# Kernel tuning notes

Measured on AMD Instinct MI355X. Metric: run time of the kernel, lower is better.

## Reference

```python
import jax, jax.numpy as jnp
import numpy as np

TIME_NUM, WEEK_NUM = 288, 7
HID = 32          # hid_dim
T_OUT, IN_DIM = 12, 3
RF_DIM = 64       # random_feature_dim
TAU = 1.0
EPS_RF = 1e-6
EPS_LN = 1e-5


def _make_proj(m, d, seed=0):
    """Performer random matrix: stacked rows of QR-orthogonalized dxd blocks,
    scaled by chi-distributed row norms (create_random_matrix, scaling=0)."""
    rng = np.random.RandomState(seed)
    blocks = []
    for _ in range(m // d):
        q, _ = np.linalg.qr(rng.randn(d, d))
        blocks.append(q.T)
    rem = m - (m // d) * d
    if rem > 0:
        q, _ = np.linalg.qr(rng.randn(d, d))
        blocks.append(q.T[:rem])
    mat = np.vstack(blocks)
    mult = np.linalg.norm(rng.randn(m, d), axis=1)
    return jnp.asarray((mult[:, None] * mat).astype(np.float32))


def setup_inputs() -> dict:
    key = jax.random.key(0)
    B, N = 4, 50000
    ks = iter(jax.random.split(key, 40))
    rn = lambda *s: jax.random.normal(next(ks), s, jnp.float32) * 0.1
    inp = {
        "x": jax.random.uniform(next(ks), (B, N, T_OUT, IN_DIM), jnp.float32),
        "node_emb": rn(N, HID),
        "time_emb": rn(TIME_NUM, HID),
        "week_emb": rn(WEEK_NUM, HID),
        "W_in": rn(HID, T_OUT * IN_DIM), "b_in": rn(HID),
        "W1": rn(HID, 3 * HID), "b1": rn(HID),
        "W2": rn(HID, 3 * HID), "b2": rn(HID),
        "W_reg": rn(T_OUT, 8 * HID), "b_reg": rn(T_OUT),
        "proj": _make_proj(RF_DIM, HID, 0),
    }
    for i in range(2):
        inp[f"fc_in{i}_w"] = rn(4 * HID, 4 * HID)
        inp[f"fc_in{i}_b"] = rn(4 * HID)
        inp[f"fc_out{i}_w"] = rn(4 * HID, 4 * HID)
        inp[f"fc_out{i}_b"] = rn(4 * HID)
        inp[f"ln{i}_g"] = jnp.ones(4 * HID, jnp.float32)
        inp[f"ln{i}_b"] = jnp.zeros(4 * HID, jnp.float32)
    return inp


def _rf_map(data, proj, is_query):
    # data: [B,N,H,D], proj: [M,D] -> features [B,N,H,M]
    d = data.shape[-1]
    data = data * (float(d) ** -0.25)
    ratio = 1.0 / jnp.sqrt(jnp.asarray(proj.shape[0], data.dtype))
    dash = jnp.einsum('bnhd,md->bnhm', data, proj)
    diag = jnp.sum(data * data, -1, keepdims=True) * 0.5
    mx = jnp.max(dash, -1, keepdims=True)
    if not is_query:
        mx = jnp.max(mx, 1, keepdims=True)  # also max over nodes (dim -3)
    return ratio * (jnp.exp(dash - diag - mx) + EPS_RF)


def _linear_kernel(x, q, k):
    # x: [B,N,H,D], q/k: [B,N,H,M] -> O(N) kernelized attention
    v2x = jnp.einsum('bnhm,bnhd->bhmd', k, x)
    out1 = jnp.einsum('bnhm,bhmd->bnhd', q, v2x)
    ksum = jnp.sum(k, axis=1)                       # [B,H,M]
    out2 = jnp.einsum('bnhm,bhm->bnh', q, ksum)[..., None]
    return out1 / out2


def _layernorm(h, g, b):
    mu = jnp.mean(h, -1, keepdims=True)
    var = jnp.mean((h - mu) ** 2, -1, keepdims=True)
    return (h - mu) * jax.lax.rsqrt(var + EPS_LN) * g + b


def _forward(x, node_emb, time_emb, week_emb, W_in, b_in, W1, b1, W2, b2,
             W_reg, b_reg, proj,
             fc_in0_w, fc_in0_b, fc_out0_w, fc_out0_b, ln0_g, ln0_b,
             fc_in1_w, fc_in1_b, fc_out1_w, fc_out1_b, ln1_g, ln1_b):
    B, N, T, D = x.shape
    time_idx = jnp.clip((x[:, :, -1, 1] * TIME_NUM).astype(jnp.int32), 0, TIME_NUM - 1)
    week_idx = jnp.clip(x[:, :, -1, 2].astype(jnp.int32), 0, WEEK_NUM - 1)
    te = time_emb[time_idx]                                  # [B,N,H]
    we = week_emb[week_idx]                                  # [B,N,H]
    ne = jnp.broadcast_to(node_emb[None], (B, N, HID))       # [B,N,H]
    inp = x.reshape(B, N, T * D) @ W_in.T + b_in             # 1x1 conv == matmul
    xg = jnp.concatenate([ne, te, we], -1)                   # [B,N,3H]
    h = jnp.concatenate([inp, ne, te, we], -1)               # [B,N,4H]

    inv_sqrt_tau = 1.0 / float(np.sqrt(TAU))
    nv1 = ((xg @ W1.T + b1) * inv_sqrt_tau)[:, :, None, :]   # [B,N,1,H]
    nv2 = ((xg @ W2.T + b2) * inv_sqrt_tau)[:, :, None, :]
    q = _rf_map(nv1, proj, True)                             # [B,N,1,M]
    k = _rf_map(nv2, proj, False)

    layers = [(fc_in0_w, fc_in0_b, fc_out0_w, fc_out0_b, ln0_g, ln0_b),
              (fc_in1_w, fc_in1_b, fc_out1_w, fc_out1_b, ln1_g, ln1_b)]
    h0 = h
    for wi, bi, wo, bo, g, bt in layers:
        res = h
        v = jax.nn.sigmoid(h @ wi.T + bi) * (h @ wo.T + bo)  # GLU; dropout=eval
        v = _linear_kernel(v[:, :, None, :], q, k)[:, :, 0, :]
        h = _layernorm(v + res, g, bt)

    out = jax.nn.relu(jnp.concatenate([h0, h], -1))          # [B,N,8H]
    out = out @ W_reg.T + b_reg                              # [B,N,T_out]
    return jnp.swapaxes(out, 1, 2)                           # [B,T_out,N]


def reference(x, node_emb, time_emb, week_emb, W_in, b_in, W1, b1, W2, b2,
              W_reg, b_reg, proj,
              fc_in0_w, fc_in0_b, fc_out0_w, fc_out0_b, ln0_g, ln0_b,
              fc_in1_w, fc_in1_b, fc_out1_w, fc_out1_b, ln1_g, ln1_b):
    return _forward(x, node_emb, time_emb, week_emb, W_in, b_in, W1, b1, W2, b2,
                    W_reg, b_reg, proj,
                    fc_in0_w, fc_in0_b, fc_out0_w, fc_out0_b, ln0_g, ln0_b,
                    fc_in1_w, fc_in1_b, fc_out1_w, fc_out1_b, ln1_g, ln1_b)
```

## Files before the change

### kernel.cpp

```cpp
#include <hip/hip_runtime.h>

#define NB 4
#define NN 50000
#define NT 784

#define H0B    0L
#define H1B    51200000L
#define QB     102400000L
#define KKB    128000000L
#define RMB    153600000L
#define WBFB   154400000L
#define V2F0B  154531072L
#define V2F1B  154662144L
#define KSB    154793216L
#define GMB    154794240L
#define W12B   154795264L
#define V2TB   154819840L
#define NZERO  65796

typedef short short8_t __attribute__((ext_vector_type(8)));
typedef float f32x4 __attribute__((ext_vector_type(4)));

__device__ __forceinline__ unsigned short f2bf(float f){
  unsigned u = __float_as_uint(f);
  return (unsigned short)((u + 0x7FFFu + ((u>>16)&1u)) >> 16);
}
__device__ __forceinline__ float bf2f(unsigned short s){
  return __uint_as_float(((unsigned)s)<<16);
}
__device__ __forceinline__ unsigned pk2(float a, float b){
  return (unsigned)f2bf(a) | ((unsigned)f2bf(b)<<16);
}
__device__ __forceinline__ uint4 pk8(const float* f){
  uint4 o; o.x=pk2(f[0],f[1]); o.y=pk2(f[2],f[3]);
  o.z=pk2(f[4],f[5]); o.w=pk2(f[6],f[7]); return o;
}
__device__ __forceinline__ void up8(uint4 v, float* f){
  f[0]=bf2f((unsigned short)(v.x&0xFFFFu)); f[1]=bf2f((unsigned short)(v.x>>16));
  f[2]=bf2f((unsigned short)(v.y&0xFFFFu)); f[3]=bf2f((unsigned short)(v.y>>16));
  f[4]=bf2f((unsigned short)(v.z&0xFFFFu)); f[5]=bf2f((unsigned short)(v.z>>16));
  f[6]=bf2f((unsigned short)(v.w&0xFFFFu)); f[7]=bf2f((unsigned short)(v.w>>16));
}
__device__ __forceinline__ short8_t relu8(short8_t s){
  short8_t r;
  #pragma unroll
  for (int i=0;i<8;i++){ short v = s[i]; r[i] = (v & (short)0x8000) ? (short)0 : v; }
  return r;
}
__device__ __forceinline__ unsigned encOrd(float f){
  unsigned u = __float_as_uint(f);
  return (u & 0x80000000u) ? ~u : (u | 0x80000000u);
}
__device__ __forceinline__ float decOrd(unsigned u){
  return (u & 0x80000000u) ? __uint_as_float(u & 0x7fffffffu)
                           : __uint_as_float(~u);
}

__global__ void k_init(char* __restrict__ wsb){
  int i = blockIdx.x*256 + threadIdx.x;
  if (i < NZERO) ((unsigned*)(wsb + V2F0B))[i] = 0u;
}
__global__ void k_wcvt(const float* __restrict__ wi0, const float* __restrict__ wo0,
                       const float* __restrict__ wi1, const float* __restrict__ wo1,
                       char* __restrict__ wsb){
  int idx = blockIdx.x*256 + threadIdx.x;
  if (idx >= 65536) return;
  int l = idx >> 15, r = (idx >> 7) & 255, c = idx & 127;
  const float* src = (l==0) ? ((r<128)? wi0 : wo0) : ((r<128)? wi1 : wo1);
  float v = src[(r&127)*128 + c];
  ((unsigned short*)(wsb + WBFB))[l*32768 + r*128 + c] = f2bf(v);
}
__global__ void k_wcvt2(const float* __restrict__ W1, const float* __restrict__ W2,
                        const float* __restrict__ proj, const float* __restrict__ W_reg,
                        char* __restrict__ wsb){
  int i = blockIdx.x*256 + threadIdx.x;
  if (i >= 12288) return;
  unsigned short* dst = (unsigned short*)(wsb + W12B);
  float v;
  if (i < 3072) v = W1[i];
  else if (i < 6144) v = W2[i-3072];
  else if (i < 8192) v = proj[i-6144];
  else {
    int r = (i-8192) >> 8, c = (i-8192) & 255;
    v = (r < 12) ? W_reg[r*256 + c] : 0.f;
  }
  dst[i] = f2bf(v);
}

__global__ __launch_bounds__(256) void k_pass1a(
  const float* __restrict__ x, const float* __restrict__ node_emb,
  const float* __restrict__ time_emb, const float* __restrict__ week_emb,
  const float* __restrict__ W_in, const float* __restrict__ b_in,
  char* __restrict__ wsb)
{
  const int b = blockIdx.y;
  const int n = blockIdx.x*256 + threadIdx.x;
  if (n >= NN) return;
  const long row = (long)b*NN + n;
  float xr[36];
  {
    const float4* xp = (const float4*)(x + row*36);
    #pragma unroll
    for (int i=0;i<9;i++){ float4 t=xp[i]; xr[4*i]=t.x; xr[4*i+1]=t.y; xr[4*i+2]=t.z; xr[4*i+3]=t.w; }
  }
  int tidx = (int)(xr[34]*288.0f); tidx = tidx<0?0:(tidx>287?287:tidx);
  int widx = (int)(xr[35]);        widx = widx<0?0:(widx>6?6:widx);
  uint4* h0q = (uint4*)(wsb + H0B) + row*16;
  float hh[32];
  #pragma unroll 1
  for (int jj=0;jj<8;jj++){
    #pragma unroll
    for (int jl=0;jl<4;jl++){
      const int j = jj*4+jl;
      const float* w = W_in + j*36;
      float a0=0.f,a1=0.f,a2=0.f,a3=0.f;
      #pragma unroll
      for (int i=0;i<36;i+=4){ a0+=xr[i]*w[i]; a1+=xr[i+1]*w[i+1]; a2+=xr[i+2]*w[i+2]; a3+=xr[i+3]*w[i+3]; }
      hh[j] = b_in[j] + ((a0+a1)+(a2+a3));
    }
  }
  #pragma unroll
  for (int c=0;c<4;c++) h0q[c] = pk8(hh + 8*c);
  float xg[96];
  {
    const float4* p0 = (const float4*)(node_emb + (long)n*32);
    const float4* p1 = (const float4*)(time_emb + (long)tidx*32);
    const float4* p2 = (const float4*)(week_emb + (long)widx*32);
    #pragma unroll
    for (int i=0;i<8;i++){ float4 t=p0[i]; xg[4*i]=t.x; xg[4*i+1]=t.y; xg[4*i+2]=t.z; xg[4*i+3]=t.w; }
    #pragma unroll
    for (int i=0;i<8;i++){ float4 t=p1[i]; xg[32+4*i]=t.x; xg[32+4*i+1]=t.y; xg[32+4*i+2]=t.z; xg[32+4*i+3]=t.w; }
    #pragma unroll
    for (int i=0;i<8;i++){ float4 t=p2[i]; xg[64+4*i]=t.x; xg[64+4*i+1]=t.y; xg[64+4*i+2]=t.z; xg[64+4*i+3]=t.w; }
  }
  #pragma unroll
  for (int c=0;c<12;c++) h0q[4+c] = pk8(xg + 8*c);
}

__global__ __launch_bounds__(256) void k_pass1b(
  const float* __restrict__ b1, const float* __restrict__ b2,
  char* __restrict__ wsb)
{
  __shared__ unsigned short xgt[64][104];
  __shared__ unsigned short dt[2][64][40];
  __shared__ unsigned short ot[64][72];
  __shared__ float wred[4];
  const int b   = blockIdx.y;
  const int tid = threadIdx.x;
  const int lane= tid & 63;
  const int w   = tid >> 6;
  const int c   = lane & 15;
  const int kg  = lane >> 4;
  const long r0blk = (long)blockIdx.x * 64;
  {
    int row = tid >> 2, q3 = tid & 3;
    long gr = r0blk + row;
    uint4 v0={0,0,0,0}, v1=v0, v2=v0;
    if (gr < NN){
      const uint4* src = (const uint4*)(wsb + H0B + ((long)b*NN + gr)*256 + 64 + q3*48);
      v0=src[0]; v1=src[1]; v2=src[2];
    }
    uint4* d = (uint4*)&xgt[row][q3*24];
    d[0]=v0; d[1]=v1; d[2]=v2;
  }
  __syncthreads();
  const unsigned short* w1bf = (const unsigned short*)(wsb + W12B);
  const unsigned short* w2bf = w1bf + 3072;
  const unsigned short* pjbf = w1bf + 6144;
  f32x4 accd[2][2];
  #pragma unroll
  for (int s=0;s<2;s++)
    #pragma unroll
    for (int f=0;f<2;f++) accd[s][f] = (f32x4){0.f,0.f,0.f,0.f};
  #pragma unroll
  for (int ks=0;ks<3;ks++){
    short8_t a = *(const short8_t*)&xgt[w*16 + c][ks*32 + kg*8];
    #pragma unroll
    for (int f=0;f<2;f++){
      short8_t bw1 = *(const short8_t*)(w1bf + (f*16+c)*96 + ks*32 + kg*8);
      accd[0][f] = __builtin_amdgcn_mfma_f32_16x16x32_bf16(a, bw1, accd[0][f], 0,0,0);
      short8_t bw2 = *(const short8_t*)(w2bf + (f*16+c)*96 + ks*32 + kg*8);
      accd[1][f] = __builtin_amdgcn_mfma_f32_16x16x32_bf16(a, bw2, accd[1][f], 0,0,0);
    }
  }
  const float DSC = 0.42044820762685725f;
  float dv[2][2][4];
  #pragma unroll
  for (int f=0;f<2;f++){
    float bb1 = b1[f*16+c], bb2 = b2[f*16+c];
    #pragma unroll
    for (int jj=0;jj<4;jj++){
      dv[0][f][jj] = (accd[0][f][jj] + bb1) * DSC;
      dv[1][f][jj] = (accd[1][f][jj] + bb2) * DSC;
    }
  }
  float dg[2][4];
  #pragma unroll
  for (int s=0;s<2;s++)
    #pragma unroll
    for (int jj=0;jj<4;jj++){
      float t = dv[s][0][jj]*dv[s][0][jj] + dv[s][1][jj]*dv[s][1][jj];
      #pragma unroll
      for (int off=1; off<16; off<<=1) t += __shfl_xor(t, off);
      dg[s][jj] = 0.5f * t;
    }
  #pragma unroll
  for (int s=0;s<2;s++)
    #pragma unroll
    for (int f=0;f<2;f++)
      #pragma unroll
      for (int jj=0;jj<4;jj++)
        dt[s][w*16 + kg*4 + jj][f*16 + c] = f2bf(dv[s][f][jj]);
  __syncthreads();
  f32x4 acc2[2][4];
  #pragma unroll
  for (int s=0;s<2;s++){
    short8_t ad = *(const short8_t*)&dt[s][w*16 + c][kg*8];
    #pragma unroll
    for (int f=0;f<4;f++){
      short8_t bp = *(const short8_t*)(pjbf + (f*16+c)*32 + kg*8);
      acc2[s][f] = __builtin_amdgcn_mfma_f32_16x16x32_bf16(ad, bp, (f32x4){0.f,0.f,0.f,0.f}, 0,0,0);
    }
  }
  float mx[2][4];
  #pragma unroll
  for (int s=0;s<2;s++)
    #pragma unroll
    for (int jj=0;jj<4;jj++){
      float t = fmaxf(fmaxf(acc2[s][0][jj],acc2[s][1][jj]),
                      fmaxf(acc2[s][2][jj],acc2[s][3][jj]));
      #pragma unroll
      for (int off=1; off<16; off<<=1) t = fmaxf(t, __shfl_xor(t, off));
      mx[s][jj] = t;
    }
  #pragma unroll
  for (int f=0;f<4;f++)
    #pragma unroll
    for (int jj=0;jj<4;jj++){
      float qv = 0.125f*(__expf(acc2[0][f][jj] - dg[0][jj] - mx[0][jj]) + 1e-6f);
      ot[w*16 + kg*4 + jj][f*16 + c] = f2bf(qv);
    }
  __syncthreads();
  {
    int row = tid >> 2, q3 = tid & 3;
    long gr = r0blk + row;
    if (gr < NN){
      const uint4* s = (const uint4*)&ot[row][q3*16];
      uint4* dst = (uint4*)((unsigned short*)(wsb + QB) + ((long)b*NN + gr)*64 + q3*16);
      dst[0] = s[0]; dst[1] = s[1];
    }
  }
  __syncthreads();
  float bmax = -3.0e38f;
  #pragma unroll
  for (int f=0;f<4;f++)
    #pragma unroll
    for (int jj=0;jj<4;jj++){
      float kv = __expf(acc2[1][f][jj] - mx[1][jj]);
      ot[w*16 + kg*4 + jj][f*16 + c] = f2bf(kv);
    }
  #pragma unroll
  for (int jj=0;jj<4;jj++){
    long gr = r0blk + w*16 + kg*4 + jj;
    bool val = (gr < NN);
    if (val && c==0)
      ((float*)(wsb + RMB))[(long)b*NN + gr] = mx[1][jj] - dg[1][jj];
    if (val) bmax = fmaxf(bmax, mx[1][jj]);
  }
  #pragma unroll
  for (int off=32; off>0; off>>=1) bmax = fmaxf(bmax, __shfl_xor(bmax, off));
  if (lane==0) wred[w] = bmax;
  __syncthreads();
  {
    int row = tid >> 2, q3 = tid & 3;
    long gr = r0blk + row;
    if (gr < NN){
      const uint4* s = (const uint4*)&ot[row][q3*16];
      uint4* dst = (uint4*)((unsigned short*)(wsb + KKB) + ((long)b*NN + gr)*64 + q3*16);
      dst[0] = s[0]; dst[1] = s[1];
    }
  }
  if (tid==0){
    float m2 = fmaxf(fmaxf(wred[0],wred[1]), fmaxf(wred[2],wred[3]));
    atomicMax((unsigned*)(wsb + GMB) + b, encOrd(m2));
  }
}

__global__ __launch_bounds__(256) void k_glured(
  char* __restrict__ wsb, const unsigned short* __restrict__ hsrc,
  const unsigned short* __restrict__ wbf,
  const float* __restrict__ bi, const float* __restrict__ bo,
  float* __restrict__ v2x_out, float* __restrict__ ksout)
{
  __shared__ unsigned short pool[9216];
  __shared__ unsigned short ktl[64][72];
  __shared__ float red[256];
  unsigned short (*ht)[136] = (unsigned short(*)[136])pool;
  unsigned short (*htT)[72] = (unsigned short(*)[72])pool;
  const int b = blockIdx.y;
  const int tid = threadIdx.x;
  const int lane = tid & 63;
  const int w = tid >> 6;
  const int c = lane & 15;
  const int kg = lane >> 4;
  const int nblk = gridDim.x;
  const float gm = decOrd(((const unsigned*)(wsb + GMB))[b]);
  const float* rm = (const float*)(wsb + RMB) + (long)b*NN;
  const uint4* kbase = (const uint4*)(wsb + KKB) + (long)b*NN*8;
  f32x4 racc[8];
  #pragma unroll
  for (int f=0;f<8;f++) racc[f] = (f32x4){0.f,0.f,0.f,0.f};
  float ksacc = 0.f;
  float bi_l[8], bo_l[8];
  #pragma unroll
  for (int f=0;f<8;f++){ bi_l[f] = bi[f*16+c]; bo_l[f] = bo[f*16+c]; }
  const int krr = tid>>3, kcc = tid&7;
  const int srow = tid>>2, sq3 = tid&3;
  const int rswz = ((w*16 + c) >> 3) & 7;
  uint4 hv0,hv1,hv2,hv3, krA,krB; float rmA,rmB;
  {
    const long r0 = (long)blockIdx.x*64;
    long gr = r0 + srow;
    hv0=(uint4){0,0,0,0}; hv1=hv0; hv2=hv0; hv3=hv0;
    if (gr < NN){
      const uint4* s = (const uint4*)(hsrc + ((long)b*NN + gr)*128 + sq3*32);
      hv0=s[0]; hv1=s[1]; hv2=s[2]; hv3=s[3];
    }
    krA=(uint4){0,0,0,0}; krB=krA; rmA=0.f; rmB=0.f;
    long gA = r0 + krr;      if (gA < NN){ krA = kbase[gA*8 + kcc]; rmA = rm[gA]; }
    long gB = r0 + krr + 32; if (gB < NN){ krB = kbase[gB*8 + kcc]; rmB = rm[gB]; }
  }
  #pragma unroll 1
  for (int tile = blockIdx.x; tile < NT; tile += nblk){
    const long r0 = (long)tile*64;
    {
      uint4* d = (uint4*)&ht[srow][sq3*32];
      d[0]=hv0; d[1]=hv1; d[2]=hv2; d[3]=hv3;
    }
    {
      bool vA = (r0 + krr) < NN;
      bool vB = (r0 + krr + 32) < NN;
      float sA = __expf(rmA - gm), sB = __expf(rmB - gm);
      float ta[8], tb[8];
      up8(krA, ta); up8(krB, tb);
      #pragma unroll
      for (int i=0;i<8;i++){
        ta[i] = vA ? 0.125f*(ta[i]*sA + 1e-6f) : 0.f;
        tb[i] = vB ? 0.125f*(tb[i]*sB + 1e-6f) : 0.f;
      }
      const int pA = (((krr>>3) ^ kcc) << 3) | (krr & 7);
      const int pB = ((((krr>>3)+4) ^ kcc) << 3) | (krr & 7);
      #pragma unroll
      for (int i=0;i<8;i++){
        ktl[kcc*8+i][pA] = f2bf(ta[i]);
        ktl[kcc*8+i][pB] = f2bf(tb[i]);
      }
    }
    if (tile + nblk < NT){
      const long r1 = (long)(tile + nblk)*64;
      long gr = r1 + srow;
      hv0=(uint4){0,0,0,0}; hv1=hv0; hv2=hv0; hv3=hv0;
      if (gr < NN){
        const uint4* s = (const uint4*)(hsrc + ((long)b*NN + gr)*128 + sq3*32);
        hv0=s[0]; hv1=s[1]; hv2=s[2]; hv3=s[3];
      }
      krA=(uint4){0,0,0,0}; krB=krA; rmA=0.f; rmB=0.f;
      long gA = r1 + krr;      if (gA < NN){ krA = kbase[gA*8 + kcc]; rmA = rm[gA]; }
      long gB = r1 + krr + 32; if (gB < NN){ krB = kbase[gB*8 + kcc]; rmB = rm[gB]; }
    }
    __syncthreads();
    f32x4 gacc[16];
    #pragma unroll
    for (int f=0;f<16;f++) gacc[f] = (f32x4){0.f,0.f,0.f,0.f};
    #pragma unroll
    for (int ks=0;ks<4;ks++){
      short8_t a = *(const short8_t*)&ht[w*16 + c][ks*32 + kg*8];
      #pragma unroll
      for (int f=0;f<16;f++){
        short8_t bb = *(const short8_t*)(wbf + (f*16 + c)*128 + ks*32 + kg*8);
        gacc[f] = __builtin_amdgcn_mfma_f32_16x16x32_bf16(a, bb, gacc[f], 0, 0, 0);
      }
    }
    float ov[8][4];
    #pragma unroll
    for (int f=0;f<8;f++)
      #pragma unroll
      for (int j=0;j<4;j++){
        float aa = gacc[f][j]   + bi_l[f];
        float cc2= gacc[f+8][j] + bo_l[f];
        ov[f][j] = cc2 / (1.0f + __expf(-aa));
      }
    if (ksout){
      int m = tid & 63, n0 = (tid>>6)*16;
      int sm = (m>>3)&7;
      #pragma unroll
      for (int n=0;n<16;n++){
        int nn = n0+n;
        ksacc += bf2f(ktl[m][(((nn>>3)^sm)<<3)|(nn&7)]);
      }
    }
    __syncthreads();
    #pragma unroll
    for (int f=0;f<8;f++)
      #pragma unroll
      for (int j=0;j<4;j++){
        bool val = (r0 + w*16 + kg*4 + j) < NN;
        htT[f*16 + c][w*16 + kg*4 + j] = val ? f2bf(ov[f][j]) : (unsigned short)0;
      }
    __syncthreads();
    #pragma unroll
    for (int ks=0;ks<2;ks++){
      short8_t a = *(const short8_t*)&ktl[w*16 + c][((ks*4 + kg) ^ rswz) << 3];
      #pragma unroll
      for (int f=0;f<8;f++){
        short8_t bb = *(const short8_t*)&htT[f*16 + c][ks*32 + kg*8];
        racc[f] = __builtin_amdgcn_mfma_f32_16x16x32_bf16(a, bb, racc[f], 0, 0, 0);
      }
    }
    __syncthreads();
  }
  float* v2x = v2x_out + (long)b*8192;
  #pragma unroll
  for (int f=0;f<8;f++)
    #pragma unroll
    for (int j=0;j<4;j++)
      atomicAdd(&v2x[(w*16 + kg*4 + j)*128 + f*16 + c], racc[f][j]);
  if (ksout){
    red[tid] = ksacc;
    __syncthreads();
    if (tid < 64)
      atomicAdd(ksout + b*64 + tid,
                red[tid]+red[64+tid]+red[128+tid]+red[192+tid]);
  }
}

__global__ void k_v2cvt(char* __restrict__ wsb, const float* __restrict__ v2f){
  int idx = blockIdx.x*256 + threadIdx.x;
  if (idx >= 36864) return;
  int b = idx / 9216, rem = idx % 9216;
  int n = rem / 64, m = rem % 64;
  const float* ks = (const float*)(wsb + KSB);
  float v = (n < 128) ? v2f[b*8192 + m*128 + n] : ((n==128) ? ks[b*64+m] : 0.f);
  ((unsigned short*)(wsb + V2TB))[b*9216 + n*64 + m] = f2bf(v);
}

__global__ __launch_bounds__(256) void k_attnln(
  char* __restrict__ wsb, const float* __restrict__ g0,
  const float* __restrict__ bt0)
{
  __shared__ unsigned short ht[64][132];
  __shared__ unsigned short v2s[144*72];
  const int b = blockIdx.y;
  const int tid = threadIdx.x;
  const int lane = tid & 63;
  const int w  = tid >> 6;
  const int c  = lane & 15;
  const int kg = lane >> 4;
  const int nblk = gridDim.x;
  const int rrow = tid>>2, rq3 = tid&3;
  const unsigned short* qb = (const unsigned short*)(wsb + QB) + (long)b*NN*64;
  const unsigned short* h0g = (const unsigned short*)(wsb + H0B) + (long)b*NN*128;
  unsigned short* h1g = (unsigned short*)(wsb + H1B) + (long)b*NN*128;
  {
    const uint4* v2g = (const uint4*)((const unsigned short*)(wsb + V2TB) + b*9216);
    #pragma unroll
    for (int e=0;e<5;e++){
      int j = tid + 256*e;
      if (j < 1152){
        int row = j >> 3, cc = j & 7;
        *(uint4*)&v2s[row*72 + cc*8] = v2g[j];
      }
    }
  }
  short8_t aq0, aq1;
  uint4 rh0, rh1, rh2, rh3;
  {
    const long r0 = (long)blockIdx.x*64;
    if (r0 + w*16 + c < NN){
      const unsigned short* qrow = qb + (r0 + w*16 + c)*64 + kg*8;
      aq0 = *(const short8_t*)qrow; aq1 = *(const short8_t*)(qrow + 32);
    } else { aq0 = (short8_t){0,0,0,0,0,0,0,0}; aq1 = aq0; }
    rh0=(uint4){0,0,0,0}; rh1=rh0; rh2=rh0; rh3=rh0;
    if (r0 + rrow < NN){
      const uint4* hs = (const uint4*)(h0g + (r0 + rrow)*128 + rq3*32);
      rh0=hs[0]; rh1=hs[1]; rh2=hs[2]; rh3=hs[3];
    }
  }
  __syncthreads();
  #pragma unroll 1
  for (int tile = blockIdx.x; tile < NT; tile += nblk){
    const long r0blk = (long)tile*64;
    const long rgr = r0blk + rrow;
    f32x4 acc[9];
    #pragma unroll
    for (int f=0;f<9;f++) acc[f] = (f32x4){0.f,0.f,0.f,0.f};
    #pragma unroll
    for (int f=0;f<9;f++){
      short8_t b0 = *(const short8_t*)&v2s[(f*16 + c)*72 + kg*8];
      acc[f] = __builtin_amdgcn_mfma_f32_16x16x32_bf16(aq0, b0, acc[f], 0, 0, 0);
      short8_t b1v = *(const short8_t*)&v2s[(f*16 + c)*72 + 32 + kg*8];
      acc[f] = __builtin_amdgcn_mfma_f32_16x16x32_bf16(aq1, b1v, acc[f], 0, 0, 0);
    }
    float inv[4];
    #pragma unroll
    for (int j=0;j<4;j++) inv[j] = 1.0f / __shfl(acc[8][j], (lane & 48));
    #pragma unroll
    for (int f=0;f<8;f++)
      #pragma unroll
      for (int j=0;j<4;j++)
        ht[w*16 + kg*4 + j][f*16 + c] = f2bf(acc[f][j]*inv[j]);
    __syncthreads();
    short8_t aq0n, aq1n;
    uint4 nh0, nh1, nh2, nh3;
    {
      aq0n = (short8_t){0,0,0,0,0,0,0,0}; aq1n = aq0n;
      nh0=(uint4){0,0,0,0}; nh1=nh0; nh2=nh0; nh3=nh0;
      if (tile + nblk < NT){
        const long r1 = (long)(tile + nblk)*64;
        if (r1 + w*16 + c < NN){
          const unsigned short* qrow = qb + (r1 + w*16 + c)*64 + kg*8;
          aq0n = *(const short8_t*)qrow; aq1n = *(const short8_t*)(qrow + 32);
        }
        if (r1 + rrow < NN){
          const uint4* hs = (const uint4*)(h0g + (r1 + rrow)*128 + rq3*32);
          nh0=hs[0]; nh1=hs[1]; nh2=hs[2]; nh3=hs[3];
        }
      }
    }
    {
      float tv[32];
      {
        const uint4* os = (const uint4*)&ht[rrow][rq3*32];
        uint4 o0=os[0],o1=os[1],o2=os[2],o3=os[3];
        up8(o0,tv); up8(o1,tv+8); up8(o2,tv+16); up8(o3,tv+24);
      }
      {
        float hv[32];
        up8(rh0,hv); up8(rh1,hv+8); up8(rh2,hv+16); up8(rh3,hv+24);
        #pragma unroll
        for (int i=0;i<32;i++) tv[i] += hv[i];
      }
      float s = 0.f;
      #pragma unroll
      for (int i=0;i<32;i++) s += tv[i];
      s += __shfl_xor(s, 1); s += __shfl_xor(s, 2);
      float mu = s * (1.0f/128.0f);
      float vv = 0.f;
      #pragma unroll
      for (int i=0;i<32;i++){ float e = tv[i]-mu; vv += e*e; }
      vv += __shfl_xor(vv, 1); vv += __shfl_xor(vv, 2);
      float rs = rsqrtf(vv * (1.0f/128.0f) + 1e-5f);
      const float4* gp = (const float4*)(g0 + rq3*32);
      const float4* bp = (const float4*)(bt0 + rq3*32);
      float h1v[32];
      #pragma unroll
      for (int i8=0;i8<8;i8++){
        float4 g4 = gp[i8], b4 = bp[i8];
        h1v[i8*4  ] = (tv[i8*4  ]-mu)*rs*g4.x + b4.x;
        h1v[i8*4+1] = (tv[i8*4+1]-mu)*rs*g4.y + b4.y;
        h1v[i8*4+2] = (tv[i8*4+2]-mu)*rs*g4.z + b4.z;
        h1v[i8*4+3] = (tv[i8*4+3]-mu)*rs*g4.w + b4.w;
      }
      if (rgr < NN){
        uint4 p0=pk8(h1v), p1=pk8(h1v+8), p2=pk8(h1v+16), p3=pk8(h1v+24);
        uint4* dst = (uint4*)(h1g + rgr*128 + rq3*32);
        dst[0]=p0; dst[1]=p1; dst[2]=p2; dst[3]=p3;
      }
    }
    __syncthreads();
    aq0=aq0n; aq1=aq1n; rh0=nh0; rh1=nh1; rh2=nh2; rh3=nh3;
  }
}

__global__ __launch_bounds__(256) void k_attnhead(
  char* __restrict__ wsb, const float* __restrict__ g1,
  const float* __restrict__ bt1, const float* __restrict__ b_reg,
  float* __restrict__ out)
{
  __shared__ unsigned short ht[64][132];
  __shared__ unsigned short v2s[144*72];
  __shared__ unsigned short h0t[64][136];
  const int b = blockIdx.y;
  const int tid = threadIdx.x;
  const int lane = tid & 63;
  const int w  = tid >> 6;
  const int c  = lane & 15;
  const int kg = lane >> 4;
  const int nblk = gridDim.x;
  const int rrow = tid>>2, rq3 = tid&3;
  const unsigned short* qb  = (const unsigned short*)(wsb + QB) + (long)b*NN*64;
  const unsigned short* h0g = (const unsigned short*)(wsb + H0B) + (long)b*NN*128;
  const unsigned short* h1g = (const unsigned short*)(wsb + H1B) + (long)b*NN*128;
  {
    const uint4* v2g = (const uint4*)((const unsigned short*)(wsb + V2TB) + b*9216);
    #pragma unroll
    for (int e=0;e<5;e++){
      int j = tid + 256*e;
      if (j < 1152){
        int row = j >> 3, cc = j & 7;
        *(uint4*)&v2s[row*72 + cc*8] = v2g[j];
      }
    }
  }
  short8_t aq0, aq1;
  uint4 rh0, rh1, rh2, rh3, ah0, ah1, ah2, ah3;
  {
    const long r0 = (long)blockIdx.x*64;
    if (r0 + w*16 + c < NN){
      const unsigned short* qrow = qb + (r0 + w*16 + c)*64 + kg*8;
      aq0 = *(const short8_t*)qrow; aq1 = *(const short8_t*)(qrow + 32);
    } else { aq0 = (short8_t){0,0,0,0,0,0,0,0}; aq1 = aq0; }
    rh0=(uint4){0,0,0,0}; rh1=rh0; rh2=rh0; rh3=rh0;
    ah0=rh0; ah1=rh0; ah2=rh0; ah3=rh0;
    if (r0 + rrow < NN){
      const uint4* hs = (const uint4*)(h1g + (r0 + rrow)*128 + rq3*32);
      rh0=hs[0]; rh1=hs[1]; rh2=hs[2]; rh3=hs[3];
      const uint4* h0s = (const uint4*)(h0g + (r0 + rrow)*128 + rq3*32);
      ah0=h0s[0]; ah1=h0s[1]; ah2=h0s[2]; ah3=h0s[3];
    }
  }
  __syncthreads();
  #pragma unroll 1
  for (int tile = blockIdx.x; tile < NT; tile += nblk){
    const long r0blk = (long)tile*64;
    const long r0w = r0blk + w*16;
    const long rgr = r0blk + rrow;
    f32x4 acc[9];
    #pragma unroll
    for (int f=0;f<9;f++) acc[f] = (f32x4){0.f,0.f,0.f,0.f};
    #pragma unroll
    for (int f=0;f<9;f++){
      short8_t b0 = *(const short8_t*)&v2s[(f*16 + c)*72 + kg*8];
      acc[f] = __builtin_amdgcn_mfma_f32_16x16x32_bf16(aq0, b0, acc[f], 0, 0, 0);
      short8_t b1v = *(const short8_t*)&v2s[(f*16 + c)*72 + 32 + kg*8];
      acc[f] = __builtin_amdgcn_mfma_f32_16x16x32_bf16(aq1, b1v, acc[f], 0, 0, 0);
    }
    float inv[4];
    #pragma unroll
    for (int j=0;j<4;j++) inv[j] = 1.0f / __shfl(acc[8][j], (lane & 48));
    #pragma unroll
    for (int f=0;f<8;f++)
      #pragma unroll
      for (int j=0;j<4;j++)
        ht[w*16 + kg*4 + j][f*16 + c] = f2bf(acc[f][j]*inv[j]);
    __syncthreads();
    short8_t aq0n, aq1n;
    uint4 nh0, nh1, nh2, nh3, na0, na1, na2, na3;
    {
      aq0n = (short8_t){0,0,0,0,0,0,0,0}; aq1n = aq0n;
      nh0=(uint4){0,0,0,0}; nh1=nh0; nh2=nh0; nh3=nh0;
      na0=nh0; na1=nh0; na2=nh0; na3=nh0;
      if (tile + nblk < NT){
        const long r1 = (long)(tile + nblk)*64;
        if (r1 + w*16 + c < NN){
          const unsigned short* qrow = qb + (r1 + w*16 + c)*64 + kg*8;
          aq0n = *(const short8_t*)qrow; aq1n = *(const short8_t*)(qrow + 32);
        }
        if (r1 + rrow < NN){
          const uint4* hs = (const uint4*)(h1g + (r1 + rrow)*128 + rq3*32);
          nh0=hs[0]; nh1=hs[1]; nh2=hs[2]; nh3=hs[3];
          const uint4* h0s = (const uint4*)(h0g + (r1 + rrow)*128 + rq3*32);
          na0=h0s[0]; na1=h0s[1]; na2=h0s[2]; na3=h0s[3];
        }
      }
    }
    {
      uint4* hd = (uint4*)&h0t[rrow][rq3*32];
      hd[0]=ah0; hd[1]=ah1; hd[2]=ah2; hd[3]=ah3;
      float tv[32];
      {
        const uint4* os = (const uint4*)&ht[rrow][rq3*32];
        uint4 o0=os[0],o1=os[1],o2=os[2],o3=os[3];
        up8(o0,tv); up8(o1,tv+8); up8(o2,tv+16); up8(o3,tv+24);
      }
      {
        float hv[32];
        up8(rh0,hv); up8(rh1,hv+8); up8(rh2,hv+16); up8(rh3,hv+24);
        #pragma unroll
        for (int i=0;i<32;i++) tv[i] += hv[i];
      }
      float s = 0.f;
      #pragma unroll
      for (int i=0;i<32;i++) s += tv[i];
      s += __shfl_xor(s, 1); s += __shfl_xor(s, 2);
      float mu = s * (1.0f/128.0f);
      float vv = 0.f;
      #pragma unroll
      for (int i=0;i<32;i++){ float e = tv[i]-mu; vv += e*e; }
      vv += __shfl_xor(vv, 1); vv += __shfl_xor(vv, 2);
      float rs = rsqrtf(vv * (1.0f/128.0f) + 1e-5f);
      const float4* gp = (const float4*)(g1 + rq3*32);
      const float4* bp = (const float4*)(bt1 + rq3*32);
      float h2v[32];
      #pragma unroll
      for (int i8=0;i8<8;i8++){
        float4 g4 = gp[i8], b4 = bp[i8];
        h2v[i8*4  ] = fmaxf((tv[i8*4  ]-mu)*rs*g4.x + b4.x, 0.f);
        h2v[i8*4+1] = fmaxf((tv[i8*4+1]-mu)*rs*g4.y + b4.y, 0.f);
        h2v[i8*4+2] = fmaxf((tv[i8*4+2]-mu)*rs*g4.z + b4.z, 0.f);
        h2v[i8*4+3] = fmaxf((tv[i8*4+3]-mu)*rs*g4.w + b4.w, 0.f);
      }
      uint4 p0=pk8(h2v), p1=pk8(h2v+8), p2=pk8(h2v+16), p3=pk8(h2v+24);
      uint4* d = (uint4*)&ht[rrow][rq3*32];
      d[0]=p0; d[1]=p1; d[2]=p2; d[3]=p3;
    }
    __syncthreads();
    const unsigned short* wregT = (const unsigned short*)(wsb + W12B) + 8192;
    f32x4 hacc = (f32x4){0.f,0.f,0.f,0.f};
    #pragma unroll
    for (int ks=0;ks<8;ks++){
      short8_t a;
      if (ks < 4)
        a = relu8(*(const short8_t*)&h0t[w*16 + c][ks*32 + kg*8]);
      else
        a = *(const short8_t*)&ht[w*16 + c][(ks-4)*32 + kg*8];
      short8_t bb = *(const short8_t*)(wregT + c*256 + ks*32 + kg*8);
      hacc = __builtin_amdgcn_mfma_f32_16x16x32_bf16(a, bb, hacc, 0, 0, 0);
    }
    if (c < 12){
      float br = b_reg[c];
      #pragma unroll
      for (int j=0;j<4;j++){
        long gr = r0w + kg*4 + j;
        if (gr < NN)
          out[((long)b*12 + c)*NN + gr] = hacc[j] + br;
      }
    }
    __syncthreads();
    aq0=aq0n; aq1=aq1n;
    rh0=nh0; rh1=nh1; rh2=nh2; rh3=nh3;
    ah0=na0; ah1=na1; ah2=na2; ah3=na3;
  }
}

extern "C" void kernel_launch(void* const* d_in, const int* in_sizes, int n_in,
                              void* d_out, int out_size, void* d_ws, size_t ws_size,
                              hipStream_t stream)
{
  const float* x        = (const float*)d_in[0];
  const float* node_emb = (const float*)d_in[1];
  const float* time_emb = (const float*)d_in[2];
  const float* week_emb = (const float*)d_in[3];
  const float* W_in     = (const float*)d_in[4];
  const float* b_in     = (const float*)d_in[5];
  const float* W1       = (const float*)d_in[6];
  const float* b1       = (const float*)d_in[7];
  const float* W2       = (const float*)d_in[8];
  const float* b2       = (const float*)d_in[9];
  const float* W_reg    = (const float*)d_in[10];
  const float* b_reg    = (const float*)d_in[11];
  const float* proj     = (const float*)d_in[12];
  const float* fc_in0_w = (const float*)d_in[13];
  const float* fc_in0_b = (const float*)d_in[14];
  const float* fc_out0_w= (const float*)d_in[15];
  const float* fc_out0_b= (const float*)d_in[16];
  const float* ln0_g    = (const float*)d_in[17];
  const float* ln0_b    = (const float*)d_in[18];
  const float* fc_in1_w = (const float*)d_in[19];
  const float* fc_in1_b = (const float*)d_in[20];
  const float* fc_out1_w= (const float*)d_in[21];
  const float* fc_out1_b= (const float*)d_in[22];
  const float* ln1_g    = (const float*)d_in[23];
  const float* ln1_b    = (const float*)d_in[24];
  char* wsb  = (char*)d_ws;
  float* out = (float*)d_out;

  dim3 rowgrid((NN+255)/256, NB);
  dim3 atngrid(782, NB);
  dim3 pgrid(128, NB);
  dim3 cvtgrid(144);

  k_init  <<<258, 256, 0, stream>>>(wsb);
  k_wcvt  <<<256, 256, 0, stream>>>(fc_in0_w, fc_out0_w, fc_in1_w, fc_out1_w, wsb);
  k_wcvt2 <<<48, 256, 0, stream>>>(W1, W2, proj, W_reg, wsb);
  k_pass1a<<<rowgrid, 256, 0, stream>>>(x, node_emb, time_emb, week_emb,
                                        W_in, b_in, wsb);
  k_pass1b<<<atngrid, 256, 0, stream>>>(b1, b2, wsb);
  k_glured<<<pgrid, 256, 0, stream>>>(wsb, (const unsigned short*)(wsb + H0B),
                                      (const unsigned short*)(wsb + WBFB),
                                      fc_in0_b, fc_out0_b,
                                      (float*)(wsb + V2F0B), (float*)(wsb + KSB));
  k_v2cvt <<<cvtgrid, 256, 0, stream>>>(wsb, (const float*)(wsb + V2F0B));
  k_attnln<<<pgrid, 256, 0, stream>>>(wsb, ln0_g, ln0_b);
  k_glured<<<pgrid, 256, 0, stream>>>(wsb, (const unsigned short*)(wsb + H1B),
                                      (const unsigned short*)(wsb + WBFB) + 32768,
                                      fc_in1_b, fc_out1_b,
                                      (float*)(wsb + V2F1B), (float*)nullptr);
  k_v2cvt <<<cvtgrid, 256, 0, stream>>>(wsb, (const float*)(wsb + V2F1B));
  k_attnhead<<<pgrid, 256, 0, stream>>>(wsb, ln1_g, ln1_b, b_reg, out);
}
```

Measured before the change: 383.2 us.

## Make pass1b persistent with register prefetch; double-buffer ktl in glured to drop barriers

```diff
diff --git a/kernel.cpp b/kernel.cpp
--- a/kernel.cpp
+++ b/kernel.cpp
@@ -151,138 +151,154 @@
   const int w   = tid >> 6;
   const int c   = lane & 15;
   const int kg  = lane >> 4;
-  const long r0blk = (long)blockIdx.x * 64;
-  {
-    int row = tid >> 2, q3 = tid & 3;
-    long gr = r0blk + row;
-    uint4 v0={0,0,0,0}, v1=v0, v2=v0;
-    if (gr < NN){
-      const uint4* src = (const uint4*)(wsb + H0B + ((long)b*NN + gr)*256 + 64 + q3*48);
-      v0=src[0]; v1=src[1]; v2=src[2];
-    }
-    uint4* d = (uint4*)&xgt[row][q3*24];
-    d[0]=v0; d[1]=v1; d[2]=v2;
-  }
-  __syncthreads();
+  const int nblk = gridDim.x;
+  const int srow = tid >> 2, sq3 = tid & 3;
   const unsigned short* w1bf = (const unsigned short*)(wsb + W12B);
   const unsigned short* w2bf = w1bf + 3072;
   const unsigned short* pjbf = w1bf + 6144;
-  f32x4 accd[2][2];
-  #pragma unroll
-  for (int s=0;s<2;s++)
-    #pragma unroll
-    for (int f=0;f<2;f++) accd[s][f] = (f32x4){0.f,0.f,0.f,0.f};
-  #pragma unroll
-  for (int ks=0;ks<3;ks++){
-    short8_t a = *(const short8_t*)&xgt[w*16 + c][ks*32 + kg*8];
+  uint4 xv0, xv1, xv2;
+  {
+    const long r0 = (long)blockIdx.x*64;
+    long gr = r0 + srow;
+    xv0=(uint4){0,0,0,0}; xv1=xv0; xv2=xv0;
+    if (gr < NN){
+      const uint4* src = (const uint4*)(wsb + H0B + ((long)b*NN + gr)*256 + 64 + sq3*48);
+      xv0=src[0]; xv1=src[1]; xv2=src[2];
+    }
+  }
+  #pragma unroll 1
+  for (int tile = blockIdx.x; tile < NT; tile += nblk){
+    const long r0blk = (long)tile*64;
+    {
+      uint4* d = (uint4*)&xgt[srow][sq3*24];
+      d[0]=xv0; d[1]=xv1; d[2]=xv2;
+    }
+    if (tile + nblk < NT){
+      const long r1 = (long)(tile + nblk)*64;
+      long gr = r1 + srow;
+      xv0=(uint4){0,0,0,0}; xv1=xv0; xv2=xv0;
+      if (gr < NN){
+        const uint4* src = (const uint4*)(wsb + H0B + ((long)b*NN + gr)*256 + 64 + sq3*48);
+        xv0=src[0]; xv1=src[1]; xv2=src[2];
+      }
+    }
+    __syncthreads();
+    f32x4 accd[2][2];
+    #pragma unroll
+    for (int s=0;s<2;s++)
+      #pragma unroll
+      for (int f=0;f<2;f++) accd[s][f] = (f32x4){0.f,0.f,0.f,0.f};
+    #pragma unroll
+    for (int ks=0;ks<3;ks++){
+      short8_t a = *(const short8_t*)&xgt[w*16 + c][ks*32 + kg*8];
+      #pragma unroll
+      for (int f=0;f<2;f++){
+        short8_t bw1 = *(const short8_t*)(w1bf + (f*16+c)*96 + ks*32 + kg*8);
+        accd[0][f] = __builtin_amdgcn_mfma_f32_16x16x32_bf16(a, bw1, accd[0][f], 0,0,0);
+        short8_t bw2 = *(const short8_t*)(w2bf + (f*16+c)*96 + ks*32 + kg*8);
+        accd[1][f] = __builtin_amdgcn_mfma_f32_16x16x32_bf16(a, bw2, accd[1][f], 0,0,0);
+      }
+    }
+    const float DSC = 0.42044820762685725f;
+    float dv[2][2][4];
     #pragma unroll
     for (int f=0;f<2;f++){
-      short8_t bw1 = *(const short8_t*)(w1bf + (f*16+c)*96 + ks*32 + kg*8);
-      accd[0][f] = __builtin_amdgcn_mfma_f32_16x16x32_bf16(a, bw1, accd[0][f], 0,0,0);
-      short8_t bw2 = *(const short8_t*)(w2bf + (f*16+c)*96 + ks*32 + kg*8);
-      accd[1][f] = __builtin_amdgcn_mfma_f32_16x16x32_bf16(a, bw2, accd[1][f], 0,0,0);
-    }
-  }
-  const float DSC = 0.42044820762685725f;
-  float dv[2][2][4];
-  #pragma unroll
-  for (int f=0;f<2;f++){
-    float bb1 = b1[f*16+c], bb2 = b2[f*16+c];
+      float bb1 = b1[f*16+c], bb2 = b2[f*16+c];
+      #pragma unroll
+      for (int jj=0;jj<4;jj++){
+        dv[0][f][jj] = (accd[0][f][jj] + bb1) * DSC;
+        dv[1][f][jj] = (accd[1][f][jj] + bb2) * DSC;
+      }
+    }
+    float dg[2][4];
+    #pragma unroll
+    for (int s=0;s<2;s++)
+      #pragma unroll
+      for (int jj=0;jj<4;jj++){
+        float t = dv[s][0][jj]*dv[s][0][jj] + dv[s][1][jj]*dv[s][1][jj];
+        #pragma unroll
+        for (int off=1; off<16; off<<=1) t += __shfl_xor(t, off);
+        dg[s][jj] = 0.5f * t;
+      }
+    #pragma unroll
+    for (int s=0;s<2;s++)
+      #pragma unroll
+      for (int f=0;f<2;f++)
+        #pragma unroll
+        for (int jj=0;jj<4;jj++)
+          dt[s][w*16 + kg*4 + jj][f*16 + c] = f2bf(dv[s][f][jj]);
+    __syncthreads();
+    f32x4 acc2[2][4];
+    #pragma unroll
+    for (int s=0;s<2;s++){
+      short8_t ad = *(const short8_t*)&dt[s][w*16 + c][kg*8];
+      #pragma unroll
+      for (int f=0;f<4;f++){
+        short8_t bp = *(const short8_t*)(pjbf + (f*16+c)*32 + kg*8);
+        acc2[s][f] = __builtin_amdgcn_mfma_f32_16x16x32_bf16(ad, bp, (f32x4){0.f,0.f,0.f,0.f}, 0,0,0);
+      }
+    }
+    float mx[2][4];
+    #pragma unroll
+    for (int s=0;s<2;s++)
+      #pragma unroll
+      for (int jj=0;jj<4;jj++){
+        float t = fmaxf(fmaxf(acc2[s][0][jj],acc2[s][1][jj]),
+                        fmaxf(acc2[s][2][jj],acc2[s][3][jj]));
+        #pragma unroll
+        for (int off=1; off<16; off<<=1) t = fmaxf(t, __shfl_xor(t, off));
+        mx[s][jj] = t;
+      }
+    #pragma unroll
+    for (int f=0;f<4;f++)
+      #pragma unroll
+      for (int jj=0;jj<4;jj++){
+        float qv = 0.125f*(__expf(acc2[0][f][jj] - dg[0][jj] - mx[0][jj]) + 1e-6f);
+        ot[w*16 + kg*4 + jj][f*16 + c] = f2bf(qv);
+      }
+    __syncthreads();
+    {
+      long gr = r0blk + srow;
+      if (gr < NN){
+        const uint4* s = (const uint4*)&ot[srow][sq3*16];
+        uint4* dst = (uint4*)((unsigned short*)(wsb + QB) + ((long)b*NN + gr)*64 + sq3*16);
+        dst[0] = s[0]; dst[1] = s[1];
+      }
+    }
+    __syncthreads();
+    float bmax = -3.0e38f;
+    #pragma unroll
+    for (int f=0;f<4;f++)
+      #pragma unroll
+      for (int jj=0;jj<4;jj++){
+        float kv = __expf(acc2[1][f][jj] - mx[1][jj]);
+        ot[w*16 + kg*4 + jj][f*16 + c] = f2bf(kv);
+      }
     #pragma unroll
     for (int jj=0;jj<4;jj++){
-      dv[0][f][jj] = (accd[0][f][jj] + bb1) * DSC;
-      dv[1][f][jj] = (accd[1][f][jj] + bb2) * DSC;
-    }
-  }
-  float dg[2][4];
-  #pragma unroll
-  for (int s=0;s<2;s++)
-    #pragma unroll
-    for (int jj=0;jj<4;jj++){
-      float t = dv[s][0][jj]*dv[s][0][jj] + dv[s][1][jj]*dv[s][1][jj];
-      #pragma unroll
-      for (int off=1; off<16; off<<=1) t += __shfl_xor(t, off);
-      dg[s][jj] = 0.5f * t;
-    }
-  #pragma unroll
-  for (int s=0;s<2;s++)
-    #pragma unroll
-    for (int f=0;f<2;f++)
-      #pragma unroll
-      for (int jj=0;jj<4;jj++)
-        dt[s][w*16 + kg*4 + jj][f*16 + c] = f2bf(dv[s][f][jj]);
-  __syncthreads();
-  f32x4 acc2[2][4];
-  #pragma unroll
-  for (int s=0;s<2;s++){
-    short8_t ad = *(const short8_t*)&dt[s][w*16 + c][kg*8];
-    #pragma unroll
-    for (int f=0;f<4;f++){
-      short8_t bp = *(const short8_t*)(pjbf + (f*16+c)*32 + kg*8);
-      acc2[s][f] = __builtin_amdgcn_mfma_f32_16x16x32_bf16(ad, bp, (f32x4){0.f,0.f,0.f,0.f}, 0,0,0);
-    }
-  }
-  float mx[2][4];
-  #pragma unroll
-  for (int s=0;s<2;s++)
-    #pragma unroll
-    for (int jj=0;jj<4;jj++){
-      float t = fmaxf(fmaxf(acc2[s][0][jj],acc2[s][1][jj]),
-                      fmaxf(acc2[s][2][jj],acc2[s][3][jj]));
-      #pragma unroll
-      for (int off=1; off<16; off<<=1) t = fmaxf(t, __shfl_xor(t, off));
-      mx[s][jj] = t;
-    }
-  #pragma unroll
-  for (int f=0;f<4;f++)
-    #pragma unroll
-    for (int jj=0;jj<4;jj++){
-      float qv = 0.125f*(__expf(acc2[0][f][jj] - dg[0][jj] - mx[0][jj]) + 1e-6f);
-      ot[w*16 + kg*4 + jj][f*16 + c] = f2bf(qv);
-    }
-  __syncthreads();
-  {
-    int row = tid >> 2, q3 = tid & 3;
-    long gr = r0blk + row;
-    if (gr < NN){
-      const uint4* s = (const uint4*)&ot[row][q3*16];
-      uint4* dst = (uint4*)((unsigned short*)(wsb + QB) + ((long)b*NN + gr)*64 + q3*16);
-      dst[0] = s[0]; dst[1] = s[1];
-    }
-  }
-  __syncthreads();
-  float bmax = -3.0e38f;
-  #pragma unroll
-  for (int f=0;f<4;f++)
-    #pragma unroll
-    for (int jj=0;jj<4;jj++){
-      float kv = __expf(acc2[1][f][jj] - mx[1][jj]);
-      ot[w*16 + kg*4 + jj][f*16 + c] = f2bf(kv);
-    }
-  #pragma unroll
-  for (int jj=0;jj<4;jj++){
-    long gr = r0blk + w*16 + kg*4 + jj;
-    bool val = (gr < NN);
-    if (val && c==0)
-      ((float*)(wsb + RMB))[(long)b*NN + gr] = mx[1][jj] - dg[1][jj];
-    if (val) bmax = fmaxf(bmax, mx[1][jj]);
-  }
-  #pragma unroll
-  for (int off=32; off>0; off>>=1) bmax = fmaxf(bmax, __shfl_xor(bmax, off));
-  if (lane==0) wred[w] = bmax;
-  __syncthreads();
-  {
-    int row = tid >> 2, q3 = tid & 3;
-    long gr = r0blk + row;
-    if (gr < NN){
-      const uint4* s = (const uint4*)&ot[row][q3*16];
-      uint4* dst = (uint4*)((unsigned short*)(wsb + KKB) + ((long)b*NN + gr)*64 + q3*16);
-      dst[0] = s[0]; dst[1] = s[1];
-    }
-  }
-  if (tid==0){
-    float m2 = fmaxf(fmaxf(wred[0],wred[1]), fmaxf(wred[2],wred[3]));
-    atomicMax((unsigned*)(wsb + GMB) + b, encOrd(m2));
+      long gr = r0blk + w*16 + kg*4 + jj;
+      bool val = (gr < NN);
+      if (val && c==0)
+        ((float*)(wsb + RMB))[(long)b*NN + gr] = mx[1][jj] - dg[1][jj];
+      if (val) bmax = fmaxf(bmax, mx[1][jj]);
+    }
+    #pragma unroll
+    for (int off=32; off>0; off>>=1) bmax = fmaxf(bmax, __shfl_xor(bmax, off));
+    if (lane==0) wred[w] = bmax;
+    __syncthreads();
+    {
+      long gr = r0blk + srow;
+      if (gr < NN){
+        const uint4* s = (const uint4*)&ot[srow][sq3*16];
+        uint4* dst = (uint4*)((unsigned short*)(wsb + KKB) + ((long)b*NN + gr)*64 + sq3*16);
+        dst[0] = s[0]; dst[1] = s[1];
+      }
+    }
+    if (tid==0){
+      float m2 = fmaxf(fmaxf(wred[0],wred[1]), fmaxf(wred[2],wred[3]));
+      atomicMax((unsigned*)(wsb + GMB) + b, encOrd(m2));
+    }
+    __syncthreads();
   }
 }
 
@@ -292,11 +308,10 @@
   const float* __restrict__ bi, const float* __restrict__ bo,
   float* __restrict__ v2x_out, float* __restrict__ ksout)
 {
-  __shared__ unsigned short pool[9216];
-  __shared__ unsigned short ktl[64][72];
+  __shared__ unsigned short ht[64][132];
+  __shared__ unsigned short htT[128][72];
+  __shared__ unsigned short ktl[2][64][72];
   __shared__ float red[256];
-  unsigned short (*ht)[136] = (unsigned short(*)[136])pool;
-  unsigned short (*htT)[72] = (unsigned short(*)[72])pool;
   const int b = blockIdx.y;
   const int tid = threadIdx.x;
   const int lane = tid & 63;
@@ -330,6 +345,7 @@
     long gA = r0 + krr;      if (gA < NN){ krA = kbase[gA*8 + kcc]; rmA = rm[gA]; }
     long gB = r0 + krr + 32; if (gB < NN){ krB = kbase[gB*8 + kcc]; rmB = rm[gB]; }
   }
+  int p = 0;
   #pragma unroll 1
   for (int tile = blockIdx.x; tile < NT; tile += nblk){
     const long r0 = (long)tile*64;
@@ -352,8 +368,8 @@
       const int pB = ((((krr>>3)+4) ^ kcc) << 3) | (krr & 7);
       #pragma unroll
       for (int i=0;i<8;i++){
-        ktl[kcc*8+i][pA] = f2bf(ta[i]);
-        ktl[kcc*8+i][pB] = f2bf(tb[i]);
+        ktl[p][kcc*8+i][pA] = f2bf(ta[i]);
+        ktl[p][kcc*8+i][pB] = f2bf(tb[i]);
       }
     }
     if (tile + nblk < NT){
@@ -381,14 +397,15 @@
         gacc[f] = __builtin_amdgcn_mfma_f32_16x16x32_bf16(a, bb, gacc[f], 0, 0, 0);
       }
     }
-    float ov[8][4];
     #pragma unroll
     for (int f=0;f<8;f++)
       #pragma unroll
       for (int j=0;j<4;j++){
         float aa = gacc[f][j]   + bi_l[f];
         float cc2= gacc[f+8][j] + bo_l[f];
-        ov[f][j] = cc2 / (1.0f + __expf(-aa));
+        float o  = cc2 / (1.0f + __expf(-aa));
+        bool val = (r0 + w*16 + kg*4 + j) < NN;
+        htT[f*16 + c][w*16 + kg*4 + j] = val ? f2bf(o) : (unsigned short)0;
       }
     if (ksout){
       int m = tid & 63, n0 = (tid>>6)*16;
@@ -396,28 +413,20 @@
       #pragma unroll
       for (int n=0;n<16;n++){
         int nn = n0+n;
-        ksacc += bf2f(ktl[m][(((nn>>3)^sm)<<3)|(nn&7)]);
-      }
-    }
-    __syncthreads();
-    #pragma unroll
-    for (int f=0;f<8;f++)
-      #pragma unroll
-      for (int j=0;j<4;j++){
-        bool val = (r0 + w*16 + kg*4 + j) < NN;
-        htT[f*16 + c][w*16 + kg*4 + j] = val ? f2bf(ov[f][j]) : (unsigned short)0;
-      }
+        ksacc += bf2f(ktl[p][m][(((nn>>3)^sm)<<3)|(nn&7)]);
+      }
+    }
     __syncthreads();
     #pragma unroll
     for (int ks=0;ks<2;ks++){
-      short8_t a = *(const short8_t*)&ktl[w*16 + c][((ks*4 + kg) ^ rswz) << 3];
+      short8_t a = *(const short8_t*)&ktl[p][w*16 + c][((ks*4 + kg) ^ rswz) << 3];
       #pragma unroll
       for (int f=0;f<8;f++){
         short8_t bb = *(const short8_t*)&htT[f*16 + c][ks*32 + kg*8];
         racc[f] = __builtin_amdgcn_mfma_f32_16x16x32_bf16(a, bb, racc[f], 0, 0, 0);
       }
     }
-    __syncthreads();
+    p ^= 1;
   }
   float* v2x = v2x_out + (long)b*8192;
   #pragma unroll
@@ -766,7 +775,6 @@
   float* out = (float*)d_out;
 
   dim3 rowgrid((NN+255)/256, NB);
-  dim3 atngrid(782, NB);
   dim3 pgrid(128, NB);
   dim3 cvtgrid(144);
 
@@ -775,7 +783,7 @@
   k_wcvt2 <<<48, 256, 0, stream>>>(W1, W2, proj, W_reg, wsb);
   k_pass1a<<<rowgrid, 256, 0, stream>>>(x, node_emb, time_emb, week_emb,
                                         W_in, b_in, wsb);
-  k_pass1b<<<atngrid, 256, 0, stream>>>(b1, b2, wsb);
+  k_pass1b<<<pgrid, 256, 0, stream>>>(b1, b2, wsb);
   k_glured<<<pgrid, 256, 0, stream>>>(wsb, (const unsigned short*)(wsb + H0B),
                                       (const unsigned short*)(wsb + WBFB),
                                       fc_in0_b, fc_out0_b,
```

New measurement: 383.2 us. About the same (+0.0%).
